# Performance work log

Measured on AMD Instinct MI355X. Metric: run time of the kernel, lower is better.

Reference implementation:

```python
import jax, jax.numpy as jnp
import numpy as np

N_NODES = 50000
N_EDGES = 800000
N_GRAPHS = 64
D = 90


def _kaiming_uniform(key, shape, fan_in):
    # kaiming_uniform_ with nonlinearity='relu': gain=sqrt(2), bound=gain*sqrt(3/fan_in)
    bound = np.sqrt(2.0) * np.sqrt(3.0 / fan_in)
    return jax.random.uniform(key, shape, jnp.float32, -bound, bound)


def setup_inputs() -> dict:
    key = jax.random.key(0)
    ks = jax.random.split(key, 16)
    x = jax.random.normal(ks[0], (N_NODES, D), jnp.float32)
    edge_index = jax.random.randint(ks[1], (2, N_EDGES), 0, N_NODES, jnp.int64)
    batch = jnp.sort(jax.random.randint(ks[2], (N_NODES,), 0, N_GRAPHS, jnp.int64))
    inp = {"x": x, "edge_index": edge_index, "batch": batch}
    # SAGEConv params: lin_l (neighbor path, with bias), lin_r (root path, no bias)
    for i, (kl, kr) in enumerate([(ks[3], ks[4]), (ks[5], ks[6]), (ks[7], ks[8])], start=1):
        inp[f"W{i}l"] = _kaiming_uniform(kl, (D, D), D)
        inp[f"b{i}"] = jnp.zeros((D,), jnp.float32)
        inp[f"W{i}r"] = _kaiming_uniform(kr, (D, D), D)
    inp["Wf1"] = _kaiming_uniform(ks[9], (32, D), D)
    inp["bf1"] = jnp.zeros((32,), jnp.float32)
    inp["Wf2"] = _kaiming_uniform(ks[10], (1, 32), 32)
    inp["bf2"] = jnp.zeros((1,), jnp.float32)
    return inp


def _sage_conv(x, src, dst, Wl, bl, Wr):
    # mean-aggregate neighbor messages x[src] at dst, then lin_l(agg) + lin_r(x)
    msg = x[src]                                           # [E, D] gather
    agg = jax.ops.segment_sum(msg, dst, num_segments=N_NODES)  # [N, D] scatter-add
    deg = jax.ops.segment_sum(jnp.ones((src.shape[0],), x.dtype), dst,
                              num_segments=N_NODES)
    agg = agg / jnp.maximum(deg, 1.0)[:, None]
    return agg @ Wl.T + bl + x @ Wr.T


def reference(x, edge_index, batch, W1l, b1, W1r, W2l, b2, W2r, W3l, b3, W3r,
              Wf1, bf1, Wf2, bf2):
    src, dst = edge_index[0], edge_index[1]
    h = jax.nn.relu(_sage_conv(x, src, dst, W1l, b1, W1r))
    h = jax.nn.relu(_sage_conv(h, src, dst, W2l, b2, W2r))
    h = jax.nn.relu(_sage_conv(h, src, dst, W3l, b3, W3r))
    # global_mean_pool over graph ids
    sums = jax.ops.segment_sum(h, batch, num_segments=N_GRAPHS)      # [G, D]
    cnts = jax.ops.segment_sum(jnp.ones((h.shape[0],), h.dtype), batch,
                               num_segments=N_GRAPHS)
    pooled = sums / jnp.maximum(cnts, 1.0)[:, None]
    h4 = jax.nn.relu(pooled @ Wf1.T + bf1)
    return h4 @ Wf2.T + bf2  # [G, 1]
```

## Files before the change

### kernel.cpp

```cpp
#include <hip/hip_runtime.h>
#include <hip/hip_bf16.h>

#define N_NODES 50000
#define N_PAD   50048
#define N_EDGES 800000
#define N_GRAPHS 64
#define D 90
#define HS  96
#define HSD 48
#define SC  192

#define NBUCKETS 196
#define BSHIFT 8
#define BIN_EPB 4096

typedef __attribute__((ext_vector_type(8))) short bf16x8;
typedef __attribute__((ext_vector_type(4))) float f32x4;

__device__ __forceinline__ float bflo(unsigned int v) { return __uint_as_float(v << 16); }
__device__ __forceinline__ float bfhi(unsigned int v) { return __uint_as_float(v & 0xffff0000u); }
__device__ __forceinline__ unsigned short bf16bits(float f) {
    __hip_bfloat16 b = __float2bfloat16(f);
    return *(unsigned short*)&b;
}
__device__ __forceinline__ unsigned int pack2bf(float lo, float hi) {
    return (unsigned int)bf16bits(lo) | ((unsigned int)bf16bits(hi) << 16);
}

__global__ void k_prep(const float* __restrict__ x, __hip_bfloat16* __restrict__ h0,
                       const float* __restrict__ w1l, const float* __restrict__ w1r,
                       const float* __restrict__ w2l, const float* __restrict__ w2r,
                       const float* __restrict__ w3l, const float* __restrict__ w3r,
                       __hip_bfloat16* __restrict__ Wcat,
                       int* __restrict__ bcnt, float* __restrict__ pooled) {
    int idx = blockIdx.x * 256 + threadIdx.x;
    if (idx < N_PAD * HS) {
        int n = idx / HS, k = idx - n * HS;
        float v = (n < N_NODES && k < D) ? x[n * D + k] : 0.f;
        h0[idx] = __float2bfloat16(v);
    }
    if (idx < 3 * 96 * SC) {
        const int per = 96 * SC;
        int layer = idx / per, rem = idx - layer * per;
        int j = rem / SC, k = rem - j * SC;
        const float* wl = (layer == 0) ? w1l : (layer == 1) ? w2l : w3l;
        const float* wr = (layer == 0) ? w1r : (layer == 1) ? w2r : w3r;
        float v = 0.f;
        if (j < D) {
            if (k < 96) { if (k < D) v = wl[j * D + k]; }
            else        { int kk = k - 96; if (kk < D) v = wr[j * D + kk]; }
        }
        Wcat[idx] = __float2bfloat16(v);
    }
    if (idx < N_GRAPHS * D + N_GRAPHS) pooled[idx] = 0.f;
    if (idx < NBUCKETS) bcnt[idx] = 0;
}

__global__ void k_hist(const int* __restrict__ dst, int* __restrict__ bcnt) {
    __shared__ int h[NBUCKETS];
    int t = threadIdx.x;
    for (int i = t; i < NBUCKETS; i += 256) h[i] = 0;
    __syncthreads();
    int base = blockIdx.x * BIN_EPB;
    int lim = base + BIN_EPB; if (lim > N_EDGES) lim = N_EDGES;
    for (int e = base + t; e < lim; e += 256)
        atomicAdd(&h[dst[e] >> BSHIFT], 1);
    __syncthreads();
    for (int i = t; i < NBUCKETS; i += 256) {
        int c = h[i];
        if (c) atomicAdd(&bcnt[i], c);
    }
}

__global__ void k_bscan(const int* __restrict__ bcnt, int* __restrict__ bbase,
                        int* __restrict__ bcursor) {
    __shared__ int s[256];
    int t = threadIdx.x;
    int v = (t < NBUCKETS) ? bcnt[t] : 0;
    s[t] = v; __syncthreads();
    for (int o = 1; o < 256; o <<= 1) {
        int x = (t >= o) ? s[t - o] : 0;
        __syncthreads();
        s[t] += x;
        __syncthreads();
    }
    int excl = s[t] - v;
    if (t < NBUCKETS) { bbase[t] = excl; bcursor[t] = excl; }
    if (t == 255) bbase[NBUCKETS] = s[255];
}

__global__ __launch_bounds__(256) void k_bin(const int* __restrict__ src,
                                             const int* __restrict__ dst,
                                             int* __restrict__ bcursor,
                                             unsigned int* __restrict__ ebuf) {
    __shared__ int h[NBUCKETS];
    __shared__ int gb[NBUCKETS];
    int t = threadIdx.x;
    for (int i = t; i < NBUCKETS; i += 256) h[i] = 0;
    __syncthreads();
    int base = blockIdx.x * BIN_EPB;
    int sv[16], dv[16], rv[16];
    #pragma unroll
    for (int i = 0; i < 16; ++i) {
        int e = base + i * 256 + t;
        if (e < N_EDGES) {
            sv[i] = src[e];
            dv[i] = dst[e];
            rv[i] = atomicAdd(&h[dv[i] >> BSHIFT], 1);
        }
    }
    __syncthreads();
    for (int i = t; i < NBUCKETS; i += 256)
        gb[i] = h[i] ? atomicAdd(&bcursor[i], h[i]) : 0;
    __syncthreads();
    #pragma unroll
    for (int i = 0; i < 16; ++i) {
        int e = base + i * 256 + t;
        if (e < N_EDGES) {
            int b = dv[i] >> BSHIFT;
            ebuf[gb[b] + rv[i]] = (unsigned int)sv[i] | ((unsigned int)(dv[i] & 255) << 16);
        }
    }
}

__global__ __launch_bounds__(256) void k_fill2(const unsigned int* __restrict__ ebuf,
                                               const int* __restrict__ bbase,
                                               int* __restrict__ off,
                                               int* __restrict__ csr) {
    __shared__ int lcnt[256];
    __shared__ int excl[256];
    int t = threadIdx.x;
    int n0 = blockIdx.x << BSHIFT;
    int ebeg = bbase[blockIdx.x], eend = bbase[blockIdx.x + 1];
    lcnt[t] = 0;
    __syncthreads();
    for (int e = ebeg + t; e < eend; e += 256)
        atomicAdd(&lcnt[ebuf[e] >> 16], 1);
    __syncthreads();
    int v = lcnt[t];
    excl[t] = v; __syncthreads();
    for (int o = 1; o < 256; o <<= 1) {
        int x = (t >= o) ? excl[t - o] : 0;
        __syncthreads();
        excl[t] += x;
        __syncthreads();
    }
    excl[t] -= v;
    int n = n0 + t;
    if (n <= N_NODES) off[n] = ebeg + excl[t];
    lcnt[t] = 0;
    __syncthreads();
    for (int e = ebeg + t; e < eend; e += 256) {
        unsigned int u = ebuf[e];
        int li = u >> 16;
        int r = atomicAdd(&lcnt[li], 1);
        csr[ebeg + excl[li] + r] = (int)(u & 0xFFFFu);
    }
}

__global__ __launch_bounds__(256) void k_layer(
    const unsigned int* __restrict__ hin,
    const __hip_bfloat16* __restrict__ Wcat,
    const float* __restrict__ bias,
    const int* __restrict__ off, const int* __restrict__ csr,
    __hip_bfloat16* __restrict__ hout)
{
    __shared__ unsigned int aggT[32][52];
    __shared__ float biasPad[96];
    int tid = threadIdx.x;
    if (tid < 96) biasPad[tid] = (tid < D) ? bias[tid] : 0.f;
    int w = tid >> 6, lane = tid & 63;

    int grp = lane >> 3, sl = lane & 7;
    int local = w * 8 + grp;
    int node = blockIdx.x * 32 + local;
    int colw = 6 * sl;

    int beg = 0, end = 0;
    if (node < N_NODES) { beg = off[node]; end = off[node + 1]; }

    float a[12];
    #pragma unroll
    for (int q = 0; q < 12; ++q) a[q] = 0.f;

    int e = beg;
    for (; e + 4 <= end; e += 4) {
        int s0 = csr[e], s1 = csr[e + 1], s2 = csr[e + 2], s3 = csr[e + 3];
        const unsigned int* p0 = &hin[s0 * HSD + colw];
        const unsigned int* p1 = &hin[s1 * HSD + colw];
        const unsigned int* p2 = &hin[s2 * HSD + colw];
        const unsigned int* p3 = &hin[s3 * HSD + colw];
        unsigned int u0[6], u1[6], u2[6], u3[6];
        #pragma unroll
        for (int q = 0; q < 6; ++q) u0[q] = p0[q];
        #pragma unroll
        for (int q = 0; q < 6; ++q) u1[q] = p1[q];
        #pragma unroll
        for (int q = 0; q < 6; ++q) u2[q] = p2[q];
        #pragma unroll
        for (int q = 0; q < 6; ++q) u3[q] = p3[q];
        #pragma unroll
        for (int q = 0; q < 6; ++q) {
            a[2 * q]     += (bflo(u0[q]) + bflo(u1[q])) + (bflo(u2[q]) + bflo(u3[q]));
            a[2 * q + 1] += (bfhi(u0[q]) + bfhi(u1[q])) + (bfhi(u2[q]) + bfhi(u3[q]));
        }
    }
    for (; e < end; ++e) {
        const unsigned int* p0 = &hin[csr[e] * HSD + colw];
        unsigned int u0[6];
        #pragma unroll
        for (int q = 0; q < 6; ++q) u0[q] = p0[q];
        #pragma unroll
        for (int q = 0; q < 6; ++q) {
            a[2 * q]     += bflo(u0[q]);
            a[2 * q + 1] += bfhi(u0[q]);
        }
    }

    {
        float inv = 1.0f / fmaxf((float)(end - beg), 1.0f);
        #pragma unroll
        for (int q = 0; q < 6; ++q) {
            int c0 = 12 * sl + 2 * q;
            float lo = (c0     < D) ? a[2 * q]     * inv : 0.f;
            float hi = (c0 + 1 < D) ? a[2 * q + 1] * inv : 0.f;
            aggT[local][colw + q] = pack2bf(lo, hi);
        }
    }
    __syncthreads();

    int w2 = w & 1, half = w >> 1;
    int mrow = lane & 15, kg = lane >> 4;
    int r0 = blockIdx.x * 32 + w2 * 16;
    int lrow = w2 * 16 + mrow;
    const short* Wp = (const short*)Wcat;
    const short* Hs = (const short*)hin;

    f32x4 acc[3];
    #pragma unroll
    for (int t = 0; t < 3; ++t) {
        int j = (half * 3 + t) * 16 + mrow;
        float b = biasPad[j];
        acc[t] = (f32x4){b, b, b, b};
    }

    #pragma unroll
    for (int ks = 0; ks < 6; ++ks) {
        bf16x8 afr;
        if (ks < 3) afr = *(const bf16x8*)&aggT[lrow][ks * 16 + kg * 4];
        else        afr = *(const bf16x8*)&Hs[(r0 + mrow) * HS + (ks - 3) * 32 + kg * 8];
        #pragma unroll
        for (int t = 0; t < 3; ++t) {
            int j = (half * 3 + t) * 16 + mrow;
            bf16x8 bfr = *(const bf16x8*)&Wp[j * SC + ks * 32 + kg * 8];
            acc[t] = __builtin_amdgcn_mfma_f32_16x16x32_bf16(afr, bfr, acc[t], 0, 0, 0);
        }
    }

    int orow = r0 + kg * 4;
    #pragma unroll
    for (int t = 0; t < 3; ++t) {
        int j = (half * 3 + t) * 16 + mrow;
        #pragma unroll
        for (int v = 0; v < 4; ++v) {
            float val = (j < D) ? fmaxf(acc[t][v], 0.f) : 0.f;
            hout[(orow + v) * HS + j] = __float2bfloat16(val);
        }
    }
}

#define POOL_WAVES 4096
__global__ void k_pool(const unsigned int* __restrict__ h, const int* __restrict__ batch,
                       float* __restrict__ pooled, float* __restrict__ cntg) {
    int wid  = (blockIdx.x * blockDim.x + threadIdx.x) >> 6;
    int lane = threadIdx.x & 63;
    const int per = (N_NODES + POOL_WAVES - 1) / POOL_WAVES;
    int beg = wid * per;
    int end = beg + per; if (end > N_NODES) end = N_NODES;
    if (beg >= end) return;
    int cur = batch[beg];
    float a0 = 0.f, a1 = 0.f, c = 0.f;
    for (int n = beg; n < end; ++n) {
        int g = batch[n];
        if (g != cur) {
            if (lane < 45) {
                atomicAdd(&pooled[cur * D + 2 * lane], a0);
                atomicAdd(&pooled[cur * D + 2 * lane + 1], a1);
            }
            if (lane == 0) atomicAdd(&cntg[cur], c);
            a0 = a1 = c = 0.f;
            cur = g;
        }
        if (lane < 45) {
            unsigned int v = h[n * HSD + lane];
            a0 += bflo(v);
            a1 += bfhi(v);
        }
        c += 1.f;
    }
    if (lane < 45) {
        atomicAdd(&pooled[cur * D + 2 * lane], a0);
        atomicAdd(&pooled[cur * D + 2 * lane + 1], a1);
    }
    if (lane == 0) atomicAdd(&cntg[cur], c);
}

__global__ void k_mlp(const float* __restrict__ pooled, const float* __restrict__ cntg,
                      const float* __restrict__ Wf1, const float* __restrict__ bf1,
                      const float* __restrict__ Wf2, const float* __restrict__ bf2,
                      float* __restrict__ outp) {
    __shared__ float P[N_GRAPHS][92];
    __shared__ float H4[N_GRAPHS][32];
    int tid = threadIdx.x;
    for (int idx = tid; idx < N_GRAPHS * D; idx += 256) {
        int g = idx / D, d = idx - g * D;
        P[g][d] = pooled[idx] / fmaxf(cntg[g], 1.0f);
    }
    __syncthreads();
    for (int idx = tid; idx < N_GRAPHS * 32; idx += 256) {
        int g = idx >> 5, c = idx & 31;
        float acc = bf1[c];
        for (int d = 0; d < D; ++d) acc += P[g][d] * Wf1[c * D + d];
        H4[g][c] = fmaxf(acc, 0.f);
    }
    __syncthreads();
    if (tid < N_GRAPHS) {
        float acc = bf2[0];
        #pragma unroll
        for (int c = 0; c < 32; ++c) acc += H4[tid][c] * Wf2[c];
        outp[tid] = acc;
    }
}

extern "C" void kernel_launch(void* const* d_in, const int* in_sizes, int n_in,
                              void* d_out, int out_size, void* d_ws, size_t ws_size,
                              hipStream_t stream) {
    const float* x    = (const float*)d_in[0];
    const int*   ei   = (const int*)d_in[1];
    const int*   batch= (const int*)d_in[2];
    const float* W1l  = (const float*)d_in[3];
    const float* b1   = (const float*)d_in[4];
    const float* W1r  = (const float*)d_in[5];
    const float* W2l  = (const float*)d_in[6];
    const float* b2   = (const float*)d_in[7];
    const float* W2r  = (const float*)d_in[8];
    const float* W3l  = (const float*)d_in[9];
    const float* b3   = (const float*)d_in[10];
    const float* W3r  = (const float*)d_in[11];
    const float* Wf1  = (const float*)d_in[12];
    const float* bf1  = (const float*)d_in[13];
    const float* Wf2  = (const float*)d_in[14];
    const float* bf2  = (const float*)d_in[15];
    const int* srcI = ei;
    const int* dstI = ei + N_EDGES;

    char* base = (char*)d_ws;
    size_t o = 0;
    auto alloc = [&](size_t bytes) -> void* {
        void* p = base + o;
        o = (o + bytes + 255) & ~(size_t)255;
        return p;
    };
    int*   bcnt    = (int*)alloc((size_t)NBUCKETS * 4);
    int*   bbase   = (int*)alloc((size_t)(NBUCKETS + 1) * 4);
    int*   bcursor = (int*)alloc((size_t)NBUCKETS * 4);
    int*   off     = (int*)alloc((size_t)(N_NODES + 1) * 4);
    unsigned int* ebuf = (unsigned int*)alloc((size_t)N_EDGES * 4);
    int*   csr     = (int*)alloc((size_t)N_EDGES * 4);
    __hip_bfloat16* hA = (__hip_bfloat16*)alloc((size_t)N_PAD * HS * 2);
    __hip_bfloat16* hB = (__hip_bfloat16*)alloc((size_t)N_PAD * HS * 2);
    __hip_bfloat16* Wcat = (__hip_bfloat16*)alloc((size_t)3 * 96 * SC * 2);
    float* pooled = (float*)alloc((size_t)(N_GRAPHS * D + N_GRAPHS) * 4);
    float* cntg   = pooled + N_GRAPHS * D;

    k_prep<<<(N_PAD * HS + 255) / 256, 256, 0, stream>>>(
        x, hA, W1l, W1r, W2l, W2r, W3l, W3r, Wcat, bcnt, pooled);

    const int EB = (N_EDGES + BIN_EPB - 1) / BIN_EPB;
    k_hist<<<EB, 256, 0, stream>>>(dstI, bcnt);
    k_bscan<<<1, 256, 0, stream>>>(bcnt, bbase, bcursor);
    k_bin<<<EB, 256, 0, stream>>>(srcI, dstI, bcursor, ebuf);
    k_fill2<<<NBUCKETS, 256, 0, stream>>>(ebuf, bbase, off, csr);

    const int LAYER_BLOCKS = N_PAD / 32;

    unsigned int* hAu = (unsigned int*)hA;
    unsigned int* hBu = (unsigned int*)hB;

    k_layer<<<LAYER_BLOCKS, 256, 0, stream>>>(hAu, Wcat,            b1, off, csr, hB);
    k_layer<<<LAYER_BLOCKS, 256, 0, stream>>>(hBu, Wcat +  96 * SC, b2, off, csr, hA);
    k_layer<<<LAYER_BLOCKS, 256, 0, stream>>>(hAu, Wcat + 192 * SC, b3, off, csr, hB);

    k_pool<<<POOL_WAVES / 4, 256, 0, stream>>>(hBu, batch, pooled, cntg);
    k_mlp<<<1, 256, 0, stream>>>(pooled, cntg, Wf1, bf1, Wf2, bf2, (float*)d_out);
}
```

Measured before the change: 217.4 us.

## Gather neighbor features from an FP8 copy of node features

Each layer now also writes an FP8 copy of its output, padded to 128 bytes per row, and the next layer gathers neighbour rows from that copy with one 16-byte vector load per lane instead of six dword loads of bf16. The goal is to roughly halve gather bandwidth in the edge-aggregation phase, which dominates the layer kernel. In exchange, prep and each layer write an extra buffer, and aggregation accuracy drops to FP8 precision, which risks tolerance failures. The root path and the MFMA still use the bf16 copy.

```diff
diff --git a/kernel.cpp b/kernel.cpp
--- a/kernel.cpp
+++ b/kernel.cpp
@@ -8,6 +8,7 @@
 #define D 90
 #define HS  96
 #define HSD 48
+#define H8D 32
 #define SC  192
 
 #define NBUCKETS 196
@@ -16,6 +17,8 @@
 
 typedef __attribute__((ext_vector_type(8))) short bf16x8;
 typedef __attribute__((ext_vector_type(4))) float f32x4;
+typedef __attribute__((ext_vector_type(2))) float f32x2;
+typedef __attribute__((ext_vector_type(4))) unsigned int u32x4;
 
 __device__ __forceinline__ float bflo(unsigned int v) { return __uint_as_float(v << 16); }
 __device__ __forceinline__ float bfhi(unsigned int v) { return __uint_as_float(v & 0xffff0000u); }
@@ -26,14 +29,30 @@
 __device__ __forceinline__ unsigned int pack2bf(float lo, float hi) {
     return (unsigned int)bf16bits(lo) | ((unsigned int)bf16bits(hi) << 16);
 }
+__device__ __forceinline__ unsigned char f32_to_fp8(float v) {
+    int pk = __builtin_amdgcn_cvt_pk_fp8_f32(v, v, 0, false);
+    return (unsigned char)(pk & 0xff);
+}
+__device__ __forceinline__ void acc_fp8_dword(float* a, unsigned int u) {
+    f32x2 lo = __builtin_amdgcn_cvt_pk_f32_fp8((int)u, false);
+    f32x2 hi = __builtin_amdgcn_cvt_pk_f32_fp8((int)u, true);
+    a[0] += lo.x; a[1] += lo.y; a[2] += hi.x; a[3] += hi.y;
+}
 
 __global__ void k_prep(const float* __restrict__ x, __hip_bfloat16* __restrict__ h0,
+                       unsigned char* __restrict__ h8a, unsigned char* __restrict__ h8b,
                        const float* __restrict__ w1l, const float* __restrict__ w1r,
                        const float* __restrict__ w2l, const float* __restrict__ w2r,
                        const float* __restrict__ w3l, const float* __restrict__ w3r,
                        __hip_bfloat16* __restrict__ Wcat,
                        int* __restrict__ bcnt, float* __restrict__ pooled) {
     int idx = blockIdx.x * 256 + threadIdx.x;
+    if (idx < N_PAD * 128) {
+        int n = idx >> 7, j = idx & 127;
+        float v = (n < N_NODES && j < D) ? x[n * D + j] : 0.f;
+        h8a[idx] = f32_to_fp8(v);
+        h8b[idx] = 0;
+    }
     if (idx < N_PAD * HS) {
         int n = idx / HS, k = idx - n * HS;
         float v = (n < N_NODES && k < D) ? x[n * D + k] : 0.f;
@@ -160,10 +179,12 @@
 
 __global__ __launch_bounds__(256) void k_layer(
     const unsigned int* __restrict__ hin,
+    const unsigned int* __restrict__ hin8,
     const __hip_bfloat16* __restrict__ Wcat,
     const float* __restrict__ bias,
     const int* __restrict__ off, const int* __restrict__ csr,
-    __hip_bfloat16* __restrict__ hout)
+    __hip_bfloat16* __restrict__ hout,
+    unsigned char* __restrict__ hout8)
 {
     __shared__ unsigned int aggT[32][52];
     __shared__ float biasPad[96];
@@ -174,57 +195,45 @@
     int grp = lane >> 3, sl = lane & 7;
     int local = w * 8 + grp;
     int node = blockIdx.x * 32 + local;
-    int colw = 6 * sl;
 
     int beg = 0, end = 0;
     if (node < N_NODES) { beg = off[node]; end = off[node + 1]; }
 
-    float a[12];
-    #pragma unroll
-    for (int q = 0; q < 12; ++q) a[q] = 0.f;
+    const u32x4* h8v = (const u32x4*)hin8;
+
+    float a[16];
+    #pragma unroll
+    for (int q = 0; q < 16; ++q) a[q] = 0.f;
 
     int e = beg;
     for (; e + 4 <= end; e += 4) {
-        int s0 = csr[e], s1 = csr[e + 1], s2 = csr[e + 2], s3 = csr[e + 3];
-        const unsigned int* p0 = &hin[s0 * HSD + colw];
-        const unsigned int* p1 = &hin[s1 * HSD + colw];
-        const unsigned int* p2 = &hin[s2 * HSD + colw];
-        const unsigned int* p3 = &hin[s3 * HSD + colw];
-        unsigned int u0[6], u1[6], u2[6], u3[6];
-        #pragma unroll
-        for (int q = 0; q < 6; ++q) u0[q] = p0[q];
-        #pragma unroll
-        for (int q = 0; q < 6; ++q) u1[q] = p1[q];
-        #pragma unroll
-        for (int q = 0; q < 6; ++q) u2[q] = p2[q];
-        #pragma unroll
-        for (int q = 0; q < 6; ++q) u3[q] = p3[q];
-        #pragma unroll
-        for (int q = 0; q < 6; ++q) {
-            a[2 * q]     += (bflo(u0[q]) + bflo(u1[q])) + (bflo(u2[q]) + bflo(u3[q]));
-            a[2 * q + 1] += (bfhi(u0[q]) + bfhi(u1[q])) + (bfhi(u2[q]) + bfhi(u3[q]));
-        }
+        u32x4 U0 = h8v[csr[e]     * 8 + sl];
+        u32x4 U1 = h8v[csr[e + 1] * 8 + sl];
+        u32x4 U2 = h8v[csr[e + 2] * 8 + sl];
+        u32x4 U3 = h8v[csr[e + 3] * 8 + sl];
+        #pragma unroll
+        for (int q = 0; q < 4; ++q) acc_fp8_dword(&a[4 * q], U0[q]);
+        #pragma unroll
+        for (int q = 0; q < 4; ++q) acc_fp8_dword(&a[4 * q], U1[q]);
+        #pragma unroll
+        for (int q = 0; q < 4; ++q) acc_fp8_dword(&a[4 * q], U2[q]);
+        #pragma unroll
+        for (int q = 0; q < 4; ++q) acc_fp8_dword(&a[4 * q], U3[q]);
     }
     for (; e < end; ++e) {
-        const unsigned int* p0 = &hin[csr[e] * HSD + colw];
-        unsigned int u0[6];
-        #pragma unroll
-        for (int q = 0; q < 6; ++q) u0[q] = p0[q];
-        #pragma unroll
-        for (int q = 0; q < 6; ++q) {
-            a[2 * q]     += bflo(u0[q]);
-            a[2 * q + 1] += bfhi(u0[q]);
-        }
-    }
-
-    {
+        u32x4 U0 = h8v[csr[e] * 8 + sl];
+        #pragma unroll
+        for (int q = 0; q < 4; ++q) acc_fp8_dword(&a[4 * q], U0[q]);
+    }
+
+    if (sl < 6) {
         float inv = 1.0f / fmaxf((float)(end - beg), 1.0f);
         #pragma unroll
-        for (int q = 0; q < 6; ++q) {
-            int c0 = 12 * sl + 2 * q;
+        for (int q = 0; q < 8; ++q) {
+            int c0 = 16 * sl + 2 * q;
             float lo = (c0     < D) ? a[2 * q]     * inv : 0.f;
             float hi = (c0 + 1 < D) ? a[2 * q + 1] * inv : 0.f;
-            aggT[local][colw + q] = pack2bf(lo, hi);
+            aggT[local][8 * sl + q] = pack2bf(lo, hi);
         }
     }
     __syncthreads();
@@ -265,6 +274,7 @@
         for (int v = 0; v < 4; ++v) {
             float val = (j < D) ? fmaxf(acc[t][v], 0.f) : 0.f;
             hout[(orow + v) * HS + j] = __float2bfloat16(val);
+            hout8[(orow + v) * 128 + j] = f32_to_fp8(val);
         }
     }
 }
@@ -369,12 +379,14 @@
     int*   csr     = (int*)alloc((size_t)N_EDGES * 4);
     __hip_bfloat16* hA = (__hip_bfloat16*)alloc((size_t)N_PAD * HS * 2);
     __hip_bfloat16* hB = (__hip_bfloat16*)alloc((size_t)N_PAD * HS * 2);
+    unsigned char* h8A = (unsigned char*)alloc((size_t)N_PAD * 128);
+    unsigned char* h8B = (unsigned char*)alloc((size_t)N_PAD * 128);
     __hip_bfloat16* Wcat = (__hip_bfloat16*)alloc((size_t)3 * 96 * SC * 2);
     float* pooled = (float*)alloc((size_t)(N_GRAPHS * D + N_GRAPHS) * 4);
     float* cntg   = pooled + N_GRAPHS * D;
 
-    k_prep<<<(N_PAD * HS + 255) / 256, 256, 0, stream>>>(
-        x, hA, W1l, W1r, W2l, W2r, W3l, W3r, Wcat, bcnt, pooled);
+    k_prep<<<(N_PAD * 128 + 255) / 256, 256, 0, stream>>>(
+        x, hA, h8A, h8B, W1l, W1r, W2l, W2r, W3l, W3r, Wcat, bcnt, pooled);
 
     const int EB = (N_EDGES + BIN_EPB - 1) / BIN_EPB;
     k_hist<<<EB, 256, 0, stream>>>(dstI, bcnt);
@@ -384,12 +396,14 @@
 
     const int LAYER_BLOCKS = N_PAD / 32;
 
-    unsigned int* hAu = (unsigned int*)hA;
-    unsigned int* hBu = (unsigned int*)hB;
-
-    k_layer<<<LAYER_BLOCKS, 256, 0, stream>>>(hAu, Wcat,            b1, off, csr, hB);
-    k_layer<<<LAYER_BLOCKS, 256, 0, stream>>>(hBu, Wcat +  96 * SC, b2, off, csr, hA);
-    k_layer<<<LAYER_BLOCKS, 256, 0, stream>>>(hAu, Wcat + 192 * SC, b3, off, csr, hB);
+    unsigned int* hAu  = (unsigned int*)hA;
+    unsigned int* hBu  = (unsigned int*)hB;
+    unsigned int* h8Au = (unsigned int*)h8A;
+    unsigned int* h8Bu = (unsigned int*)h8B;
+
+    k_layer<<<LAYER_BLOCKS, 256, 0, stream>>>(hAu, h8Au, Wcat,            b1, off, csr, hB, h8B);
+    k_layer<<<LAYER_BLOCKS, 256, 0, stream>>>(hBu, h8Bu, Wcat +  96 * SC, b2, off, csr, hA, h8A);
+    k_layer<<<LAYER_BLOCKS, 256, 0, stream>>>(hAu, h8Au, Wcat + 192 * SC, b3, off, csr, hB, h8B);
 
     k_pool<<<POOL_WAVES / 4, 256, 0, stream>>>(hBu, batch, pooled, cntg);
     k_mlp<<<1, 256, 0, stream>>>(pooled, cntg, Wf1, bf1, Wf2, bf2, (float*)d_out);
```

After: 200.6 us, median of 2. 7.7% less time.
